# Performance work log

Hardware: AMD Instinct MI355X
Metric: run time of the kernel (lower is better)

The kernel has to match this reference:

```python
import jax, jax.numpy as jnp
import numpy as np

M, N, D = 2048, 131072, 256

def setup_inputs() -> dict:
    key = jax.random.key(0)
    kq, kv = jax.random.split(key)
    query = jax.random.normal(kq, (M, D), dtype=jnp.float32)
    vectors = jax.random.normal(kv, (N, D), dtype=jnp.float32)
    return {"query": query, "vectors": vectors}

def reference(query, vectors):
    # torch.cdist(query, vectors, p=2).argmin(dim=1)
    # Euclidean distance via ||q||^2 + ||v||^2 - 2 q.v (GEMM-based, same math)
    q_sq = jnp.sum(query * query, axis=-1, keepdims=True)        # [M,1]
    v_sq = jnp.sum(vectors * vectors, axis=-1)                    # [N]
    cross = jnp.einsum('md,nd->mn', query, vectors)               # [M,N]
    dist_sq = jnp.maximum(q_sq + v_sq[None, :] - 2.0 * cross, 0.0)
    # sqrt is monotonic so argmin(dist) == argmin(dist_sq); take sqrt for faithfulness
    dist = jnp.sqrt(dist_sq)
    return jnp.argmin(dist, axis=1)                               # [M] int
```

## Files before the change

### kernel.cpp

```cpp
#include <hip/hip_runtime.h>
#include <hip/hip_bf16.h>

#define M 2048
#define N 131072
#define D 256

#define SLICE_G 64
#define NSLICE  (N / (SLICE_G * 16))
#define BIAS    1024.0f

typedef __attribute__((ext_vector_type(8))) _Float16 half8;
typedef __attribute__((ext_vector_type(8))) short short8;
typedef __attribute__((ext_vector_type(4))) float f32x4;
typedef unsigned long long ull;

__device__ __forceinline__ ull pack_key(float score, unsigned idx) {
    unsigned u = __float_as_uint(score);
    u = (u & 0x80000000u) ? ~u : (u | 0x80000000u);
    return ((ull)u << 32) | idx;
}

__global__ __launch_bounds__(256) void convert_fused(const float* __restrict__ v,
                                                     const float* __restrict__ q,
                                                     short* __restrict__ vf,
                                                     short* __restrict__ qf,
                                                     float* __restrict__ vsqb,
                                                     ull* __restrict__ keys) {
    __shared__ float lds[16 * 260];
    __shared__ float part[4][16];

    const int b    = blockIdx.x;
    const bool isV = (b < N / 16);
    const int g    = isV ? b : (b - N / 16);
    const float* x = isV ? v : q;
    short* xf      = isV ? vf : qf;

    const int t    = threadIdx.x;
    const int w    = t >> 6;
    const int l    = t & 63;
    const int quad = (l >> 4) & 3;
    const int tx   = l & 15;

    const float* src = x + (size_t)g * 4096;
#pragma unroll
    for (int i = 0; i < 4; ++i) {
        const int fi  = (i * 256 + t) * 4;
        const float4 f = *(const float4*)(src + fi);
        const int row = fi >> 8;
        const int col = fi & 255;
        *(float4*)&lds[row * 260 + col] = f;
    }
    __syncthreads();

    float s = 0.f;
#pragma unroll
    for (int h = 0; h < 2; ++h) {
        const int c = w + h * 4;
        float tmp[8] __attribute__((aligned(16)));
        *(float4*)&tmp[0] = *(const float4*)&lds[tx * 260 + c * 32 + quad * 8];
        *(float4*)&tmp[4] = *(const float4*)&lds[tx * 260 + c * 32 + quad * 8 + 4];
        half8 hh;
#pragma unroll
        for (int e = 0; e < 8; ++e) {
            hh[e] = (_Float16)tmp[e];
            s += tmp[e] * tmp[e];
        }
        *(short8*)(xf + ((size_t)g * 8 + c) * 512 + l * 8) = *(short8*)&hh;
    }

    if (isV) {
        s += __shfl_xor(s, 16, 64);
        s += __shfl_xor(s, 32, 64);
        if (l < 16) part[w][l] = s;
        __syncthreads();
        if (t < 16) vsqb[g * 16 + t] = part[0][t] + part[1][t] + part[2][t] + part[3][t] + BIAS;
    } else if (g == 0) {
        for (int i = t; i < 2 * M; i += 256) keys[i] = ~0ull;
    }
}

__global__ __launch_bounds__(256, 2) void dist_argmin_reg(const short* __restrict__ qf,
                                                          const short* __restrict__ vf,
                                                          const float* __restrict__ vsqb,
                                                          ull* __restrict__ keys1,
                                                          ull* __restrict__ keys2) {
    const int tid  = threadIdx.x;
    const int lane = tid & 63;
    const int w    = tid >> 6;
    const int tx   = lane & 15;
    const int quad = (lane >> 4) & 3;

    const int lb    = blockIdx.x;
    const int xcd   = lb & 7;
    const int s_    = lb >> 3;
    const int slice = xcd * 16 + (s_ >> 3);
    const int qblk  = s_ & 7;

    const int qb0 = qblk * 256 + w * 64;
    const int sg0 = slice * SLICE_G;

    half8 aq[4][8];
#pragma unroll
    for (int mt = 0; mt < 4; ++mt)
#pragma unroll
        for (int c = 0; c < 8; ++c)
            aq[mt][c] = *(const half8*)(qf + ((size_t)((qb0 >> 4) + mt) * 8 + c) * 512 + lane * 8);

    unsigned best[16];
#pragma unroll
    for (int i = 0; i < 16; ++i) best[i] = 0xFFFFFFFFu;

    const short* bp = vf + ((size_t)sg0 * 8) * 512 + lane * 8;
    const float* vp = vsqb + sg0 * 16 + tx;

    half8 bA[8], bB[8];
    float vA, vB;

    auto loadg = [&](half8* b, float& vs, int g) {
        const short* p = bp + (size_t)g * 4096;
#pragma unroll
        for (int c = 0; c < 8; ++c) b[c] = *(const half8*)(p + c * 512);
        vs = vp[g * 16];
    };
    auto compute = [&](const half8* b, float vsqr, int g) {
        f32x4 acc[4];
#pragma unroll
        for (int i = 0; i < 4; ++i) acc[i] = (f32x4){0.f, 0.f, 0.f, 0.f};
#pragma unroll
        for (int c = 0; c < 8; ++c)
#pragma unroll
            for (int mt = 0; mt < 4; ++mt)
                acc[mt] = __builtin_amdgcn_mfma_f32_16x16x32_f16(aq[mt][c], b[c], acc[mt], 0, 0, 0);
#pragma unroll
        for (int mt = 0; mt < 4; ++mt)
#pragma unroll
            for (int r = 0; r < 4; ++r) {
                const float sc = fmaf(-2.f, acc[mt][r], vsqr);
                const unsigned key = (__float_as_uint(sc) & 0xFFFFFFC0u) | (unsigned)g;
                const int sl = mt * 4 + r;
                best[sl] = key < best[sl] ? key : best[sl];
            }
    };

    loadg(bA, vA, 0);
    for (int g = 0; g < SLICE_G - 2; g += 2) {
        loadg(bB, vB, g + 1);
        compute(bA, vA, g);
        loadg(bA, vA, g + 2);
        compute(bB, vB, g + 1);
    }
    loadg(bB, vB, SLICE_G - 1);
    compute(bA, vA, SLICE_G - 2);
    compute(bB, vB, SLICE_G - 1);

#pragma unroll
    for (int mt = 0; mt < 4; ++mt)
#pragma unroll
        for (int r = 0; r < 4; ++r) {
            const int sl = mt * 4 + r;
            unsigned k = best[sl];
#pragma unroll
            for (int off = 8; off; off >>= 1) {
                const unsigned o = (unsigned)__shfl_xor((int)k, off, 16);
                k = o < k ? o : k;
            }
            const ull bal = __ballot(best[sl] == k);
            const unsigned grp = (unsigned)((bal >> (quad * 16)) & 0xFFFFull);
            const int wtx = __ffs((int)grp) - 1;
            const unsigned n = (unsigned)((sg0 + (int)(k & 63u)) * 16 + wtx);
            if (tx == 0) {
                const int row = qb0 + mt * 16 + quad * 4 + r;
                const ull key64 = ((ull)k << 32) | n;
                const ull old = atomicMin(&keys1[row], key64);
                const ull loser = (key64 < old) ? old : key64;
                if (loser != ~0ull) atomicMin(&keys2[row], loser);
            }
        }
}

__global__ __launch_bounds__(256) void rescore_kernel(const float* __restrict__ q,
                                                      const float* __restrict__ v,
                                                      const ull* __restrict__ keys1,
                                                      const ull* __restrict__ keys2,
                                                      int* __restrict__ out) {
    const int qi   = blockIdx.x * 4 + (threadIdx.x >> 6);
    const int lane = threadIdx.x & 63;
    const float4 qv = *(const float4*)(q + (size_t)qi * D + lane * 4);
    ull best = ~0ull;
    ull cand[2];
    cand[0] = keys1[qi];
    cand[1] = keys2[qi];
#pragma unroll
    for (int c = 0; c < 2; ++c) {
        if (cand[c] == ~0ull) continue;
        const unsigned idx = (unsigned)cand[c];
        const float4 vv = *(const float4*)(v + (size_t)idx * D + lane * 4);
        float s1 = vv.x * vv.x + vv.y * vv.y + vv.z * vv.z + vv.w * vv.w;
        float s2 = qv.x * vv.x + qv.y * vv.y + qv.z * vv.z + qv.w * vv.w;
#pragma unroll
        for (int off = 32; off; off >>= 1) {
            s1 += __shfl_xor(s1, off, 64);
            s2 += __shfl_xor(s2, off, 64);
        }
        const float dist = fmaf(-2.0f, s2, s1);
        const ull key = pack_key(dist, idx);
        best = best < key ? best : key;
    }
    if (lane == 0) out[qi] = (int)(unsigned)(best & 0xFFFFFFFFull);
}

extern "C" void kernel_launch(void* const* d_in, const int* in_sizes, int n_in,
                              void* d_out, int out_size, void* d_ws, size_t ws_size,
                              hipStream_t stream) {
    const float* q = (const float*)d_in[0];
    const float* v = (const float*)d_in[1];
    int* out = (int*)d_out;

    char* ws = (char*)d_ws;
    float* vsqb = (float*)ws;                ws += (size_t)N * sizeof(float);
    ull* keys1 = (ull*)ws;                   ws += (size_t)2 * M * sizeof(ull);
    ull* keys2 = keys1 + M;
    short* qf = (short*)ws;                  ws += (size_t)M * D * 2;
    short* vf = (short*)ws;

    convert_fused<<<N / 16 + M / 16, 256, 0, stream>>>(v, q, vf, qf, vsqb, keys1);

    dist_argmin_reg<<<(M / 256) * NSLICE, 256, 0, stream>>>(qf, vf, vsqb, keys1, keys2);

    rescore_kernel<<<M / 4, 256, 0, stream>>>(q, v, keys1, keys2, out);
}
```

Before: 326.5 us.

## Stage shared vector tiles in double-buffered LDS via direct global-to-LDS loads

The distance kernel now loads each vector tile once per block into a double-buffered LDS array using global_load_lds, instead of every wave loading the same tile into registers. This removes redundant global/L2 traffic across the four waves and lowers register pressure, at the cost of two block barriers per tile pair and LDS reads in the MFMA loop. The conversion kernel also drops its LDS staging and reads the fp32 inputs directly from global memory.

```diff
diff --git a/kernel.cpp b/kernel.cpp
--- a/kernel.cpp
+++ b/kernel.cpp
@@ -18,6 +18,12 @@
     unsigned u = __float_as_uint(score);
     u = (u & 0x80000000u) ? ~u : (u | 0x80000000u);
     return ((ull)u << 32) | idx;
+}
+
+__device__ __forceinline__ void gload_lds16(const void* g, void* l) {
+    __builtin_amdgcn_global_load_lds(
+        (const __attribute__((address_space(1))) void*)g,
+        (__attribute__((address_space(3))) void*)l, 16, 0, 0);
 }
 
 __global__ __launch_bounds__(256) void convert_fused(const float* __restrict__ v,
@@ -26,7 +32,6 @@
                                                      short* __restrict__ qf,
                                                      float* __restrict__ vsqb,
                                                      ull* __restrict__ keys) {
-    __shared__ float lds[16 * 260];
     __shared__ float part[4][16];
 
     const int b    = blockIdx.x;
@@ -42,23 +47,15 @@
     const int tx   = l & 15;
 
     const float* src = x + (size_t)g * 4096;
-#pragma unroll
-    for (int i = 0; i < 4; ++i) {
-        const int fi  = (i * 256 + t) * 4;
-        const float4 f = *(const float4*)(src + fi);
-        const int row = fi >> 8;
-        const int col = fi & 255;
-        *(float4*)&lds[row * 260 + col] = f;
-    }
-    __syncthreads();
-
     float s = 0.f;
 #pragma unroll
     for (int h = 0; h < 2; ++h) {
         const int c = w + h * 4;
-        float tmp[8] __attribute__((aligned(16)));
-        *(float4*)&tmp[0] = *(const float4*)&lds[tx * 260 + c * 32 + quad * 8];
-        *(float4*)&tmp[4] = *(const float4*)&lds[tx * 260 + c * 32 + quad * 8 + 4];
+        const float* p = src + tx * 256 + c * 32 + quad * 8;
+        const float4 f0 = *(const float4*)p;
+        const float4 f1 = *(const float4*)(p + 4);
+        float tmp[8] __attribute__((aligned(16))) = {f0.x, f0.y, f0.z, f0.w,
+                                                     f1.x, f1.y, f1.z, f1.w};
         half8 hh;
 #pragma unroll
         for (int e = 0; e < 8; ++e) {
@@ -84,6 +81,8 @@
                                                           const float* __restrict__ vsqb,
                                                           ull* __restrict__ keys1,
                                                           ull* __restrict__ keys2) {
+    __shared__ short bt[2][8 * 512];
+
     const int tid  = threadIdx.x;
     const int lane = tid & 63;
     const int w    = tid >> 6;
@@ -110,27 +109,30 @@
 #pragma unroll
     for (int i = 0; i < 16; ++i) best[i] = 0xFFFFFFFFu;
 
-    const short* bp = vf + ((size_t)sg0 * 8) * 512 + lane * 8;
-    const float* vp = vsqb + sg0 * 16 + tx;
-
-    half8 bA[8], bB[8];
-    float vA, vB;
-
-    auto loadg = [&](half8* b, float& vs, int g) {
-        const short* p = bp + (size_t)g * 4096;
-#pragma unroll
-        for (int c = 0; c < 8; ++c) b[c] = *(const half8*)(p + c * 512);
-        vs = vp[g * 16];
+    const short* bslice = vf + (size_t)sg0 * 8 * 512;
+    const float* vp     = vsqb + sg0 * 16 + tx;
+
+    auto stage = [&](short* buf, int g) {
+        const short* gsrc = bslice + (size_t)g * 4096;
+#pragma unroll
+        for (int i = 0; i < 2; ++i) {
+            const int seg = w * 2 + i;
+            gload_lds16(gsrc + seg * 512 + lane * 8, buf + seg * 512);
+        }
     };
-    auto compute = [&](const half8* b, float vsqr, int g) {
+
+    auto compute = [&](const short* buf, int g) {
+        const float vsqr = vp[(size_t)g * 16];
         f32x4 acc[4];
 #pragma unroll
         for (int i = 0; i < 4; ++i) acc[i] = (f32x4){0.f, 0.f, 0.f, 0.f};
 #pragma unroll
-        for (int c = 0; c < 8; ++c)
+        for (int c = 0; c < 8; ++c) {
+            const half8 bfr = *(const half8*)(buf + c * 512 + lane * 8);
 #pragma unroll
             for (int mt = 0; mt < 4; ++mt)
-                acc[mt] = __builtin_amdgcn_mfma_f32_16x16x32_f16(aq[mt][c], b[c], acc[mt], 0, 0, 0);
+                acc[mt] = __builtin_amdgcn_mfma_f32_16x16x32_f16(aq[mt][c], bfr, acc[mt], 0, 0, 0);
+        }
 #pragma unroll
         for (int mt = 0; mt < 4; ++mt)
 #pragma unroll
@@ -142,16 +144,17 @@
             }
     };
 
-    loadg(bA, vA, 0);
-    for (int g = 0; g < SLICE_G - 2; g += 2) {
-        loadg(bB, vB, g + 1);
-        compute(bA, vA, g);
-        loadg(bA, vA, g + 2);
-        compute(bB, vB, g + 1);
-    }
-    loadg(bB, vB, SLICE_G - 1);
-    compute(bA, vA, SLICE_G - 2);
-    compute(bB, vB, SLICE_G - 1);
+    stage(bt[0], 0);
+    __syncthreads();
+
+    for (int g = 0; g < SLICE_G; g += 2) {
+        stage(bt[1], g + 1);
+        compute(bt[0], g);
+        __syncthreads();
+        if (g + 2 < SLICE_G) stage(bt[0], g + 2);
+        compute(bt[1], g + 1);
+        __syncthreads();
+    }
 
 #pragma unroll
     for (int mt = 0; mt < 4; ++mt)
```

After: 326.3 us. Within noise of the previous version (-0.0%).
